# Kernel tuning notes

Hardware: AMD Instinct MI355X
Metric: run time of the kernel (lower is better)

The kernel has to match this reference:

```python
import jax, jax.numpy as jnp
import numpy as np

N_TOKEN = 267735
D_PROJ = 1024
CUTOFF_ENDS = [0, 20000, 40000, 200000, 267735]
D_EMBS = [1024, 256, 64, 16]  # d_embed // div_val**i, div_val=4
EMB_SCALE = float(D_PROJ) ** 0.5


def setup_inputs() -> dict:
    key = jax.random.key(0)
    ks = jax.random.split(key, 9)
    inp = jax.random.randint(ks[0], (8, 2048), 0, N_TOKEN)
    d = {"inp": inp}
    for i in range(4):
        size = CUTOFF_ENDS[i + 1] - CUTOFF_ENDS[i]
        de = D_EMBS[i]
        d[f"emb{i}"] = jax.random.normal(ks[1 + 2 * i], (size, de), jnp.float32) * 0.02
        d[f"proj{i}"] = jax.random.normal(ks[2 + 2 * i], (D_PROJ, de), jnp.float32) * 0.02
    return d


def reference(inp, emb0, emb1, emb2, emb3, proj0, proj1, proj2, proj3):
    embs = [emb0, emb1, emb2, emb3]
    projs = [proj0, proj1, proj2, proj3]
    flat = inp.reshape(-1)  # [T]
    out = jnp.zeros((flat.shape[0], D_PROJ), jnp.float32)
    for i in range(4):
        l, r = CUTOFF_ENDS[i], CUTOFF_ENDS[i + 1]
        mask = (flat >= l) & (flat < r)  # clusters are disjoint
        idx = jnp.clip(flat - l, 0, r - l - 1)  # in-range dummy where masked out
        # gather [T, d_emb_i] then project to [T, d_proj] (F.linear with weight [d_proj, d_emb_i])
        e = jnp.einsum('td,pd->tp', embs[i][idx], projs[i])
        out = jnp.where(mask[:, None], e, out)
    return (out * EMB_SCALE).reshape(*inp.shape, D_PROJ)
```

## Files before the change

kernel.cpp:

```cpp
#include <hip/hip_runtime.h>


#define CUT0 20000
#define CUT1 40000
#define CUT2 200000

typedef __attribute__((ext_vector_type(8))) short bf16x8;
typedef __attribute__((ext_vector_type(8))) unsigned short u16x8;
typedef __attribute__((ext_vector_type(4))) unsigned short u16x4;
typedef __attribute__((ext_vector_type(4))) float f32x4;

__device__ __forceinline__ unsigned short f2bf(float f) {
    unsigned u = __float_as_uint(f);
    u += 0x7FFFu + ((u >> 16) & 1u);
    return (unsigned short)(u >> 16);
}

__global__ __launch_bounds__(256)
void classify_kernel(const int* __restrict__ inp, unsigned* __restrict__ counters,
                     unsigned* __restrict__ lists, int T) {
    int t = blockIdx.x * 256 + threadIdx.x;
    int lane = threadIdx.x & 63;
    bool valid = (t < T);
    int id = valid ? inp[t] : 0;
    int c = -1, l = 0;
    if (valid) {
        if (id < CUT0)      { c = 0; l = 0; }
        else if (id < CUT1) { c = 1; l = CUT0; }
        else if (id < CUT2) { c = 2; l = CUT1; }
        else                { c = 3; l = CUT2; }
    }
    #pragma unroll
    for (int i = 0; i < 4; ++i) {
        unsigned long long m = __ballot(c == i);
        if (c == i) {
            int leader = __ffsll(m) - 1;
            unsigned base = 0;
            if (lane == leader) base = atomicAdd(&counters[i], (unsigned)__popcll(m));
            base = __shfl(base, leader);
            unsigned rank = (unsigned)__popcll(m & ((1ull << lane) - 1ull));
            lists[(size_t)i * T + base + rank] = ((unsigned)t << 18) | (unsigned)(id - l);
        }
    }
}

#define PITCH 72

template<int K>
__device__ __forceinline__
void tile_gemm(const float* __restrict__ emb, const float* __restrict__ proj,
               const unsigned* __restrict__ list, int count, int mtile, int ntile,
               float* __restrict__ out,
               unsigned short* E_s, unsigned short* P_s, unsigned* pk_s) {
    constexpr int KB  = (K >= 64) ? 64 : K;
    constexpr int NCH = K / KB;
    constexpr int KSTEPS = (KB + 31) / 32;

    const int m0 = mtile * 64;
    const int rows = min(64, count - m0);
    const int py = ntile * 64;
    const int tid = (int)threadIdx.x;
    const int lane = tid & 63;
    const int w  = tid >> 6;
    const int ln = lane & 15;
    const int qd = lane >> 4;
    const int sr = tid >> 2;
    const int sq = tid & 3;

    if (tid < 64) pk_s[tid] = (tid < rows) ? list[m0 + tid] : 0u;
    __syncthreads();

    f32x4 acc[4];
    #pragma unroll
    for (int ct = 0; ct < 4; ++ct) acc[ct] = (f32x4){0.f, 0.f, 0.f, 0.f};

    const size_t erow = (size_t)(pk_s[sr] & 0x3FFFFu) * K;
    const size_t prow = (size_t)(py + sr) * K;

    for (int ch = 0; ch < NCH; ++ch) {
        const int kk = ch * KB;
        if constexpr (KB == 64) {
            const float* es = emb + erow + kk + sq * 16;
            const float* ps = proj + prow + kk + sq * 16;
            float4 e0 = *(const float4*)(es);
            float4 e1 = *(const float4*)(es + 4);
            float4 e2 = *(const float4*)(es + 8);
            float4 e3 = *(const float4*)(es + 12);
            float4 p0 = *(const float4*)(ps);
            float4 p1 = *(const float4*)(ps + 4);
            float4 p2 = *(const float4*)(ps + 8);
            float4 p3 = *(const float4*)(ps + 12);
            u16x8 eh0 = {f2bf(e0.x), f2bf(e0.y), f2bf(e0.z), f2bf(e0.w),
                         f2bf(e1.x), f2bf(e1.y), f2bf(e1.z), f2bf(e1.w)};
            u16x8 eh1 = {f2bf(e2.x), f2bf(e2.y), f2bf(e2.z), f2bf(e2.w),
                         f2bf(e3.x), f2bf(e3.y), f2bf(e3.z), f2bf(e3.w)};
            u16x8 ph0 = {f2bf(p0.x), f2bf(p0.y), f2bf(p0.z), f2bf(p0.w),
                         f2bf(p1.x), f2bf(p1.y), f2bf(p1.z), f2bf(p1.w)};
            u16x8 ph1 = {f2bf(p2.x), f2bf(p2.y), f2bf(p2.z), f2bf(p2.w),
                         f2bf(p3.x), f2bf(p3.y), f2bf(p3.z), f2bf(p3.w)};
            *(u16x8*)&E_s[sr * PITCH + sq * 16]     = eh0;
            *(u16x8*)&E_s[sr * PITCH + sq * 16 + 8] = eh1;
            *(u16x8*)&P_s[sr * PITCH + sq * 16]     = ph0;
            *(u16x8*)&P_s[sr * PITCH + sq * 16 + 8] = ph1;
        } else {
            float4 e0 = *(const float4*)(emb + erow + sq * 4);
            float4 p0 = *(const float4*)(proj + prow + sq * 4);
            u16x4 eh = {f2bf(e0.x), f2bf(e0.y), f2bf(e0.z), f2bf(e0.w)};
            u16x4 ph = {f2bf(p0.x), f2bf(p0.y), f2bf(p0.z), f2bf(p0.w)};
            u16x4 z  = {0, 0, 0, 0};
            *(u16x4*)&E_s[sr * PITCH + sq * 4]      = eh;
            *(u16x4*)&E_s[sr * PITCH + 16 + sq * 4] = z;
            *(u16x4*)&P_s[sr * PITCH + sq * 4]      = ph;
            *(u16x4*)&P_s[sr * PITCH + 16 + sq * 4] = z;
        }
        __syncthreads();

        const unsigned short* ea = &E_s[(w * 16 + ln) * PITCH + qd * 8];
        const unsigned short* pb = &P_s[ln * PITCH + qd * 8];
        #pragma unroll
        for (int s = 0; s < KSTEPS; ++s) {
            bf16x8 a = *(const bf16x8*)(ea + s * 32);
            #pragma unroll
            for (int ct = 0; ct < 4; ++ct) {
                bf16x8 b = *(const bf16x8*)(pb + ct * 16 * PITCH + s * 32);
                acc[ct] = __builtin_amdgcn_mfma_f32_16x16x32_bf16(a, b, acc[ct], 0, 0, 0);
            }
        }
        __syncthreads();
    }

    #pragma unroll
    for (int ct = 0; ct < 4; ++ct) {
        #pragma unroll
        for (int r = 0; r < 4; ++r) {
            int row = w * 16 + qd * 4 + r;
            if (row < rows) {
                int t = (int)(pk_s[row] >> 18);
                out[(size_t)t * 1024 + py + ct * 16 + ln] = acc[ct][r] * 32.0f;
            }
        }
    }
    __syncthreads();
}

__global__ __launch_bounds__(256)
void gemm_fused(const float* __restrict__ emb0, const float* __restrict__ proj0,
                const float* __restrict__ emb1, const float* __restrict__ proj1,
                const float* __restrict__ emb2, const float* __restrict__ proj2,
                const float* __restrict__ emb3, const float* __restrict__ proj3,
                const unsigned* __restrict__ lists, const unsigned* __restrict__ counters,
                int T, float* __restrict__ out) {
    __shared__ unsigned short E_s[64 * PITCH];
    __shared__ unsigned short P_s[64 * PITCH];
    __shared__ unsigned pk_s[64];

    const int c0 = (int)counters[0], c1 = (int)counters[1];
    const int c2 = (int)counters[2], c3 = (int)counters[3];
    const int e0t = ((c0 + 63) >> 6) * 16;
    const int e1t = e0t + ((c1 + 63) >> 6) * 16;
    const int e2t = e1t + ((c2 + 63) >> 6) * 16;
    const int e3t = e2t + ((c3 + 63) >> 6) * 16;

    for (int tile = blockIdx.x; tile < e3t; tile += gridDim.x) {
        if (tile < e0t) {
            int lt = tile;
            tile_gemm<1024>(emb0, proj0, lists + 0 * (size_t)T, c0, lt >> 4, lt & 15, out, E_s, P_s, pk_s);
        } else if (tile < e1t) {
            int lt = tile - e0t;
            tile_gemm< 256>(emb1, proj1, lists + 1 * (size_t)T, c1, lt >> 4, lt & 15, out, E_s, P_s, pk_s);
        } else if (tile < e2t) {
            int lt = tile - e1t;
            tile_gemm<  64>(emb2, proj2, lists + 2 * (size_t)T, c2, lt >> 4, lt & 15, out, E_s, P_s, pk_s);
        } else {
            int lt = tile - e2t;
            tile_gemm<  16>(emb3, proj3, lists + 3 * (size_t)T, c3, lt >> 4, lt & 15, out, E_s, P_s, pk_s);
        }
    }
}

extern "C" void kernel_launch(void* const* d_in, const int* in_sizes, int n_in,
                              void* d_out, int out_size, void* d_ws, size_t ws_size,
                              hipStream_t stream) {
    const int*   inp   = (const int*)d_in[0];
    const float* emb0  = (const float*)d_in[1];
    const float* proj0 = (const float*)d_in[2];
    const float* emb1  = (const float*)d_in[3];
    const float* proj1 = (const float*)d_in[4];
    const float* emb2  = (const float*)d_in[5];
    const float* proj2 = (const float*)d_in[6];
    const float* emb3  = (const float*)d_in[7];
    const float* proj3 = (const float*)d_in[8];
    float* out = (float*)d_out;
    const int T = in_sizes[0];

    unsigned* counters = (unsigned*)d_ws;
    unsigned* lists    = (unsigned*)((char*)d_ws + 256);

    hipMemsetAsync(counters, 0, 16, stream);
    classify_kernel<<<dim3((T + 255) / 256), 256, 0, stream>>>(inp, counters, lists, T);

    gemm_fused<<<dim3(2048), 256, 0, stream>>>(emb0, proj0, emb1, proj1,
                                               emb2, proj2, emb3, proj3,
                                               lists, counters, T, out);
}
```

Measured before the change: 227.1 us.

## Pre-convert projections and gathered embeddings to bf16, then stream into LDS directly

The conversion kernel now also turns all projection matrices into bf16 once, with the 16-wide cluster padded to 32. A new kernel gathers the selected embedding rows into a compact bf16 buffer per cluster. The GEMM then loads tiles straight from global memory into LDS with swizzled global_load_lds, uses 64x128 tiles, and assigns tiles with XCD awareness. The goal is to stop re-reading fp32 projections and redoing the bf16 conversion in every tile. The cost is extra workspace, an extra kernel launch and a bf16 intermediate round trip.

```diff
diff --git a/kernel.cpp b/kernel.cpp
--- a/kernel.cpp
+++ b/kernel.cpp
@@ -5,9 +5,13 @@
 #define CUT1 40000
 #define CUT2 200000
 
+#define PB1 (1024 * 1024)
+#define PB2 (PB1 + 1024 * 256)
+#define PB3 (PB2 + 1024 * 64)
+#define PBEND (PB3 + 1024 * 32)
+
 typedef __attribute__((ext_vector_type(8))) short bf16x8;
 typedef __attribute__((ext_vector_type(8))) unsigned short u16x8;
-typedef __attribute__((ext_vector_type(4))) unsigned short u16x4;
 typedef __attribute__((ext_vector_type(4))) float f32x4;
 
 __device__ __forceinline__ unsigned short f2bf(float f) {
@@ -16,9 +20,25 @@
     return (unsigned short)(u >> 16);
 }
 
+__device__ __forceinline__ u16x8 cvt8(const float* __restrict__ s) {
+    float4 a = *(const float4*)s;
+    float4 b = *(const float4*)(s + 4);
+    return (u16x8){f2bf(a.x), f2bf(a.y), f2bf(a.z), f2bf(a.w),
+                   f2bf(b.x), f2bf(b.y), f2bf(b.z), f2bf(b.w)};
+}
+
+__device__ __forceinline__ void gl_lds16(const unsigned short* g, unsigned short* s) {
+    __builtin_amdgcn_global_load_lds(
+        (const __attribute__((address_space(1))) void*)g,
+        (__attribute__((address_space(3))) void*)s, 16, 0, 0);
+}
+
 __global__ __launch_bounds__(256)
-void classify_kernel(const int* __restrict__ inp, unsigned* __restrict__ counters,
-                     unsigned* __restrict__ lists, int T) {
+void classify_convert(const int* __restrict__ inp, unsigned* __restrict__ counters,
+                      unsigned* __restrict__ lists, int T,
+                      const float* __restrict__ proj0, const float* __restrict__ proj1,
+                      const float* __restrict__ proj2, const float* __restrict__ proj3,
+                      unsigned short* __restrict__ projbf) {
     int t = blockIdx.x * 256 + threadIdx.x;
     int lane = threadIdx.x & 63;
     bool valid = (t < T);
@@ -42,87 +62,115 @@
             lists[(size_t)i * T + base + rank] = ((unsigned)t << 18) | (unsigned)(id - l);
         }
     }
-}
-
-#define PITCH 72
-
-template<int K>
+    const int stride = gridDim.x * 256;
+    for (int u = t; u < PBEND / 8; u += stride) {
+        int base = u * 8;
+        u16x8 o;
+        if (base < PB1)       o = cvt8(proj0 + base);
+        else if (base < PB2)  o = cvt8(proj1 + (base - PB1));
+        else if (base < PB3)  o = cvt8(proj2 + (base - PB2));
+        else {
+            int rel = base - PB3;
+            int row = rel >> 5, col = rel & 31;
+            if (col < 16) o = cvt8(proj3 + row * 16 + col);
+            else          o = (u16x8){0, 0, 0, 0, 0, 0, 0, 0};
+        }
+        *(u16x8*)(projbf + base) = o;
+    }
+}
+
+__global__ __launch_bounds__(256)
+void gather_bf16(const float* __restrict__ emb0, const float* __restrict__ emb1,
+                 const float* __restrict__ emb2, const float* __restrict__ emb3,
+                 const unsigned* __restrict__ lists, const unsigned* __restrict__ counters,
+                 int T, unsigned short* __restrict__ ecomp) {
+    const int c0 = (int)counters[0], c1 = (int)counters[1];
+    const int c2 = (int)counters[2], c3 = (int)counters[3];
+    const size_t off1 = (size_t)((c0 + 63) & ~63) * 1024;
+    const size_t off2 = off1 + (size_t)((c1 + 63) & ~63) * 256;
+    const size_t off3 = off2 + (size_t)((c2 + 63) & ~63) * 64;
+    const int n0 = c0 << 7, n1 = c1 << 5, n2 = c2 << 3, n3 = c3 << 2;
+    const int total = n0 + n1 + n2 + n3;
+    const int stride = gridDim.x * 256;
+    for (int u = blockIdx.x * 256 + threadIdx.x; u < total; u += stride) {
+        int v = u;
+        if (v < n0) {
+            int r = v >> 7, j = v & 127;
+            unsigned id = lists[r] & 0x3FFFFu;
+            *(u16x8*)(ecomp + (size_t)r * 1024 + j * 8) = cvt8(emb0 + (size_t)id * 1024 + j * 8);
+        } else if ((v -= n0) < n1) {
+            int r = v >> 5, j = v & 31;
+            unsigned id = lists[T + r] & 0x3FFFFu;
+            *(u16x8*)(ecomp + off1 + (size_t)r * 256 + j * 8) = cvt8(emb1 + (size_t)id * 256 + j * 8);
+        } else if ((v -= n1) < n2) {
+            int r = v >> 3, j = v & 7;
+            unsigned id = lists[2 * T + r] & 0x3FFFFu;
+            *(u16x8*)(ecomp + off2 + (size_t)r * 64 + j * 8) = cvt8(emb2 + (size_t)id * 64 + j * 8);
+        } else {
+            v -= n2;
+            int r = v >> 2, j = v & 3;
+            unsigned id = lists[3 * T + r] & 0x3FFFFu;
+            unsigned short* d = ecomp + off3 + (size_t)r * 32 + j * 8;
+            if (j < 2) *(u16x8*)d = cvt8(emb3 + (size_t)id * 16 + j * 8);
+            else       *(u16x8*)d = (u16x8){0, 0, 0, 0, 0, 0, 0, 0};
+        }
+    }
+}
+
+template<int KP>
 __device__ __forceinline__
-void tile_gemm(const float* __restrict__ emb, const float* __restrict__ proj,
+void tile_gemm(const unsigned short* __restrict__ E, const unsigned short* __restrict__ P,
                const unsigned* __restrict__ list, int count, int mtile, int ntile,
                float* __restrict__ out,
                unsigned short* E_s, unsigned short* P_s, unsigned* pk_s) {
-    constexpr int KB  = (K >= 64) ? 64 : K;
-    constexpr int NCH = K / KB;
-    constexpr int KSTEPS = (KB + 31) / 32;
+    constexpr int KB  = (KP >= 64) ? 64 : KP;
+    constexpr int NCH = KP / KB;
+    constexpr int KST = KB / 32;
+    constexpr int CPR = KB / 8;
+    constexpr int SWZ = CPR - 1;
 
     const int m0 = mtile * 64;
     const int rows = min(64, count - m0);
-    const int py = ntile * 64;
+    const int py = ntile * 128;
     const int tid = (int)threadIdx.x;
     const int lane = tid & 63;
     const int w  = tid >> 6;
     const int ln = lane & 15;
     const int qd = lane >> 4;
-    const int sr = tid >> 2;
-    const int sq = tid & 3;
 
     if (tid < 64) pk_s[tid] = (tid < rows) ? list[m0 + tid] : 0u;
-    __syncthreads();
-
-    f32x4 acc[4];
+
+    f32x4 acc[8];
     #pragma unroll
-    for (int ct = 0; ct < 4; ++ct) acc[ct] = (f32x4){0.f, 0.f, 0.f, 0.f};
-
-    const size_t erow = (size_t)(pk_s[sr] & 0x3FFFFu) * K;
-    const size_t prow = (size_t)(py + sr) * K;
+    for (int ct = 0; ct < 8; ++ct) acc[ct] = (f32x4){0.f, 0.f, 0.f, 0.f};
+
+    const unsigned short* eb = E + (size_t)m0 * KP;
+    const unsigned short* pb = P + (size_t)py * KP;
 
     for (int ch = 0; ch < NCH; ++ch) {
-        const int kk = ch * KB;
-        if constexpr (KB == 64) {
-            const float* es = emb + erow + kk + sq * 16;
-            const float* ps = proj + prow + kk + sq * 16;
-            float4 e0 = *(const float4*)(es);
-            float4 e1 = *(const float4*)(es + 4);
-            float4 e2 = *(const float4*)(es + 8);
-            float4 e3 = *(const float4*)(es + 12);
-            float4 p0 = *(const float4*)(ps);
-            float4 p1 = *(const float4*)(ps + 4);
-            float4 p2 = *(const float4*)(ps + 8);
-            float4 p3 = *(const float4*)(ps + 12);
-            u16x8 eh0 = {f2bf(e0.x), f2bf(e0.y), f2bf(e0.z), f2bf(e0.w),
-                         f2bf(e1.x), f2bf(e1.y), f2bf(e1.z), f2bf(e1.w)};
-            u16x8 eh1 = {f2bf(e2.x), f2bf(e2.y), f2bf(e2.z), f2bf(e2.w),
-                         f2bf(e3.x), f2bf(e3.y), f2bf(e3.z), f2bf(e3.w)};
-            u16x8 ph0 = {f2bf(p0.x), f2bf(p0.y), f2bf(p0.z), f2bf(p0.w),
-                         f2bf(p1.x), f2bf(p1.y), f2bf(p1.z), f2bf(p1.w)};
-            u16x8 ph1 = {f2bf(p2.x), f2bf(p2.y), f2bf(p2.z), f2bf(p2.w),
-                         f2bf(p3.x), f2bf(p3.y), f2bf(p3.z), f2bf(p3.w)};
-            *(u16x8*)&E_s[sr * PITCH + sq * 16]     = eh0;
-            *(u16x8*)&E_s[sr * PITCH + sq * 16 + 8] = eh1;
-            *(u16x8*)&P_s[sr * PITCH + sq * 16]     = ph0;
-            *(u16x8*)&P_s[sr * PITCH + sq * 16 + 8] = ph1;
-        } else {
-            float4 e0 = *(const float4*)(emb + erow + sq * 4);
-            float4 p0 = *(const float4*)(proj + prow + sq * 4);
-            u16x4 eh = {f2bf(e0.x), f2bf(e0.y), f2bf(e0.z), f2bf(e0.w)};
-            u16x4 ph = {f2bf(p0.x), f2bf(p0.y), f2bf(p0.z), f2bf(p0.w)};
-            u16x4 z  = {0, 0, 0, 0};
-            *(u16x4*)&E_s[sr * PITCH + sq * 4]      = eh;
-            *(u16x4*)&E_s[sr * PITCH + 16 + sq * 4] = z;
-            *(u16x4*)&P_s[sr * PITCH + sq * 4]      = ph;
-            *(u16x4*)&P_s[sr * PITCH + 16 + sq * 4] = z;
+        const int k0 = ch * KB;
+        #pragma unroll
+        for (int it = 0; it < (64 * CPR) / 256; ++it) {
+            int i16 = it * 256 + tid;
+            int row = i16 / CPR, cc = (i16 % CPR) ^ (row & SWZ);
+            gl_lds16(eb + (size_t)row * KP + k0 + cc * 8, E_s + i16 * 8);
+        }
+        #pragma unroll
+        for (int it = 0; it < (128 * CPR) / 256; ++it) {
+            int i16 = it * 256 + tid;
+            int row = i16 / CPR, cc = (i16 % CPR) ^ (row & SWZ);
+            gl_lds16(pb + (size_t)row * KP + k0 + cc * 8, P_s + i16 * 8);
         }
         __syncthreads();
 
-        const unsigned short* ea = &E_s[(w * 16 + ln) * PITCH + qd * 8];
-        const unsigned short* pb = &P_s[ln * PITCH + qd * 8];
-        #pragma unroll
-        for (int s = 0; s < KSTEPS; ++s) {
-            bf16x8 a = *(const bf16x8*)(ea + s * 32);
+        const int ar = w * 16 + ln;
+        #pragma unroll
+        for (int s = 0; s < KST; ++s) {
+            bf16x8 a = *(const bf16x8*)(E_s + ar * KB + (((s * 4 + qd) ^ (ar & SWZ)) * 8));
             #pragma unroll
-            for (int ct = 0; ct < 4; ++ct) {
-                bf16x8 b = *(const bf16x8*)(pb + ct * 16 * PITCH + s * 32);
+            for (int ct = 0; ct < 8; ++ct) {
+                const int br = ct * 16 + ln;
+                bf16x8 b = *(const bf16x8*)(P_s + br * KB + (((s * 4 + qd) ^ (br & SWZ)) * 8));
                 acc[ct] = __builtin_amdgcn_mfma_f32_16x16x32_bf16(a, b, acc[ct], 0, 0, 0);
             }
         }
@@ -130,7 +178,7 @@
     }
 
     #pragma unroll
-    for (int ct = 0; ct < 4; ++ct) {
+    for (int ct = 0; ct < 8; ++ct) {
         #pragma unroll
         for (int r = 0; r < 4; ++r) {
             int row = w * 16 + qd * 4 + r;
@@ -144,37 +192,35 @@
 }
 
 __global__ __launch_bounds__(256)
-void gemm_fused(const float* __restrict__ emb0, const float* __restrict__ proj0,
-                const float* __restrict__ emb1, const float* __restrict__ proj1,
-                const float* __restrict__ emb2, const float* __restrict__ proj2,
-                const float* __restrict__ emb3, const float* __restrict__ proj3,
+void gemm_fused(const unsigned short* __restrict__ ecomp, const unsigned short* __restrict__ projbf,
                 const unsigned* __restrict__ lists, const unsigned* __restrict__ counters,
                 int T, float* __restrict__ out) {
-    __shared__ unsigned short E_s[64 * PITCH];
-    __shared__ unsigned short P_s[64 * PITCH];
+    __shared__ unsigned short E_s[64 * 64];
+    __shared__ unsigned short P_s[128 * 64];
     __shared__ unsigned pk_s[64];
 
     const int c0 = (int)counters[0], c1 = (int)counters[1];
     const int c2 = (int)counters[2], c3 = (int)counters[3];
-    const int e0t = ((c0 + 63) >> 6) * 16;
-    const int e1t = e0t + ((c1 + 63) >> 6) * 16;
-    const int e2t = e1t + ((c2 + 63) >> 6) * 16;
-    const int e3t = e2t + ((c3 + 63) >> 6) * 16;
-
-    for (int tile = blockIdx.x; tile < e3t; tile += gridDim.x) {
-        if (tile < e0t) {
-            int lt = tile;
-            tile_gemm<1024>(emb0, proj0, lists + 0 * (size_t)T, c0, lt >> 4, lt & 15, out, E_s, P_s, pk_s);
-        } else if (tile < e1t) {
-            int lt = tile - e0t;
-            tile_gemm< 256>(emb1, proj1, lists + 1 * (size_t)T, c1, lt >> 4, lt & 15, out, E_s, P_s, pk_s);
-        } else if (tile < e2t) {
-            int lt = tile - e1t;
-            tile_gemm<  64>(emb2, proj2, lists + 2 * (size_t)T, c2, lt >> 4, lt & 15, out, E_s, P_s, pk_s);
-        } else {
-            int lt = tile - e2t;
-            tile_gemm<  16>(emb3, proj3, lists + 3 * (size_t)T, c3, lt >> 4, lt & 15, out, E_s, P_s, pk_s);
-        }
+    const size_t off1 = (size_t)((c0 + 63) & ~63) * 1024;
+    const size_t off2 = off1 + (size_t)((c1 + 63) & ~63) * 256;
+    const size_t off3 = off2 + (size_t)((c2 + 63) & ~63) * 64;
+    const int g0 = (c0 + 63) >> 6;
+    const int g1 = g0 + ((c1 + 63) >> 6);
+    const int g2 = g1 + ((c2 + 63) >> 6);
+    const int g3 = g2 + ((c3 + 63) >> 6);
+
+    const int xcd = blockIdx.x & 7;
+    const int slot = blockIdx.x >> 3;
+    const int nslots = gridDim.x >> 3;
+
+    for (int i = slot; ; i += nslots) {
+        const int g = ((i >> 3) << 3) + xcd;
+        if (g >= g3) break;
+        const int nt = i & 7;
+        if (g < g0)      tile_gemm<1024>(ecomp,        projbf,       lists,         c0, g,      nt, out, E_s, P_s, pk_s);
+        else if (g < g1) tile_gemm< 256>(ecomp + off1, projbf + PB1, lists + T,     c1, g - g0, nt, out, E_s, P_s, pk_s);
+        else if (g < g2) tile_gemm<  64>(ecomp + off2, projbf + PB2, lists + 2 * T, c2, g - g1, nt, out, E_s, P_s, pk_s);
+        else             tile_gemm<  32>(ecomp + off3, projbf + PB3, lists + 3 * T, c3, g - g2, nt, out, E_s, P_s, pk_s);
     }
 }
 
@@ -195,11 +241,14 @@
 
     unsigned* counters = (unsigned*)d_ws;
     unsigned* lists    = (unsigned*)((char*)d_ws + 256);
+    size_t lists_b = ((size_t)4 * T * 4 + 255) & ~(size_t)255;
+    unsigned short* projbf = (unsigned short*)((char*)d_ws + 256 + lists_b);
+    unsigned short* ecomp  = projbf + PBEND;
 
     hipMemsetAsync(counters, 0, 16, stream);
-    classify_kernel<<<dim3((T + 255) / 256), 256, 0, stream>>>(inp, counters, lists, T);
-
-    gemm_fused<<<dim3(2048), 256, 0, stream>>>(emb0, proj0, emb1, proj1,
-                                               emb2, proj2, emb3, proj3,
-                                               lists, counters, T, out);
-}
+    classify_convert<<<dim3(256), 256, 0, stream>>>(inp, counters, lists, T,
+                                                    proj0, proj1, proj2, proj3, projbf);
+    gather_bf16<<<dim3(2048), 256, 0, stream>>>(emb0, emb1, emb2, emb3,
+                                                lists, counters, T, ecomp);
+    gemm_fused<<<dim3(1536), 256, 0, stream>>>(ecomp, projbf, lists, counters, T, out);
+}
```

Measured after the change: 212.7 us. -6.3%, faster.
